# Performance work log

Hardware: AMD Instinct MI355X
Metric: run time of the kernel (lower is better)

The kernel has to match this reference:

```python
import jax, jax.numpy as jnp
import numpy as np

# Model dims (ViT-Base @ 384)
L, H, D, HD, M, P, IMG, B, NC, CH = 12, 12, 768, 64, 3072, 16, 384, 32, 1000, 3
NPATCH = (IMG // P) ** 2  # 576
SCALE = 1.0 / np.sqrt(HD)


def setup_inputs() -> dict:
    key = jax.random.key(0)
    ks = iter(jax.random.split(key, 16))
    def n(shape, s=0.02):
        return (jax.random.normal(next(ks), shape, jnp.float32) * s).astype(jnp.float32)
    return dict(
        x=jax.random.normal(next(ks), (B, CH, IMG, IMG), jnp.float32),
        conv_w=n((D, CH, P, P)), conv_b=jnp.zeros((D,), jnp.float32),
        cls_token=jnp.zeros((1, 1, D), jnp.float32),
        pos_emb=n((1, NPATCH + 1, D), 1.0),
        ln1_g=jnp.ones((L, D), jnp.float32), ln1_b=jnp.zeros((L, D), jnp.float32),
        wqkv=n((L, H, D, 3 * HD)), bqkv=jnp.zeros((L, H, 3 * HD), jnp.float32),
        wmsa=n((L, D, D)), bmsa=jnp.zeros((L, D), jnp.float32),
        ln2_g=jnp.ones((L, D), jnp.float32), ln2_b=jnp.zeros((L, D), jnp.float32),
        lnm_g=jnp.ones((L, D), jnp.float32), lnm_b=jnp.zeros((L, D), jnp.float32),
        w1=n((L, D, M)), b1=jnp.zeros((L, M), jnp.float32),
        w2=n((L, M, D)), b2=jnp.zeros((L, D), jnp.float32),
        lnf_g=jnp.ones((D,), jnp.float32), lnf_b=jnp.zeros((D,), jnp.float32),
        whead=n((D, NC)), bhead=jnp.zeros((NC,), jnp.float32),
    )


def _ln(x, g, b, eps=1e-5):
    mu = jnp.mean(x, axis=-1, keepdims=True)
    var = jnp.mean(jnp.square(x - mu), axis=-1, keepdims=True)
    return (x - mu) * jax.lax.rsqrt(var + eps) * g + b


def _encoder_block(x, p):
    (ln1_g, ln1_b, wqkv, bqkv, wmsa, bmsa,
     ln2_g, ln2_b, lnm_g, lnm_b, w1, b1, w2, b2) = p
    b = x.shape[0]
    h = _ln(x, ln1_g, ln1_b)
    # batched per-head QKV (math identical to looping over H small Linears)
    qkv = jnp.einsum('bsd,hde->bhse', h, wqkv) + bqkv[:, None, :]  # [B,H,S,3*HD]
    q, k, v = jnp.split(qkv, 3, axis=-1)
    attn = jax.nn.softmax(jnp.einsum('bhqe,bhke->bhqk', q, k) * SCALE, axis=-1)
    o = jnp.einsum('bhqk,bhke->bhqe', attn, v)          # [B,H,S,HD]
    o = o.transpose(0, 2, 1, 3).reshape(b, -1, D)        # concat heads along feature
    msa = jnp.einsum('bsd,de->bse', o, wmsa) + bmsa
    x1 = h + msa                                          # residual around MSA (post-LN1)
    h2 = _ln(x1, ln2_g, ln2_b)
    h2 = _ln(h2, lnm_g, lnm_b)                            # MLPBlock's own LayerNorm (double LN, faithful)
    mlp = jnp.einsum('bsm,md->bsd', jax.nn.gelu(jnp.einsum('bsd,dm->bsm', h2, w1) + b1, approximate=False), w2) + b2
    return x1 + mlp, None


def reference(x, conv_w, conv_b, cls_token, pos_emb,
              ln1_g, ln1_b, wqkv, bqkv, wmsa, bmsa,
              ln2_g, ln2_b, lnm_g, lnm_b, w1, b1, w2, b2,
              lnf_g, lnf_b, whead, bhead):
    b = x.shape[0]
    # patchify conv (image divisible by patch, so F.pad is a no-op)
    t = jax.lax.conv_general_dilated(x, conv_w, (P, P), 'VALID',
                                     dimension_numbers=('NCHW', 'OIHW', 'NCHW'))
    t = t + conv_b[None, :, None, None]
    # faithful to torch .view(b, -1, embed_dim) on NCHW layout (channel-major flatten)
    t = t.reshape(b, -1, D)
    n = t.shape[1]
    t = jnp.concatenate([jnp.broadcast_to(cls_token, (b, 1, D)), t], axis=1)
    t = t + pos_emb[:, :n + 1]
    stacked = (ln1_g, ln1_b, wqkv, bqkv, wmsa, bmsa,
               ln2_g, ln2_b, lnm_g, lnm_b, w1, b1, w2, b2)
    t, _ = jax.lax.scan(_encoder_block, t, stacked)
    y = _ln(t[:, 0], lnf_g, lnf_b)
    y = jax.nn.softmax(jnp.einsum('bd,dc->bc', y, whead) + bhead, axis=-1)
    return y
```

## Files before the change

### kernel.cpp

```cpp
#include <hip/hip_runtime.h>

using f16   = _Float16;
using f16x8 = __attribute__((ext_vector_type(8))) _Float16;
using f32x4 = __attribute__((ext_vector_type(4))) float;

#define MPAD  18560
#define MREAL 18464
#define MCONV 18432
#define SEQ   577
#define SPAD  640
#define NHEAD 12
#define NBATCH 32
#define SCALE_ 0.125f

__device__ __forceinline__ void load_lds16(const void* g, void* l) {
  __builtin_amdgcn_global_load_lds(
      (const __attribute__((address_space(1))) void*)g,
      (__attribute__((address_space(3))) void*)l, 16, 0, 0);
}

template<int K, int EPI>
__global__ __launch_bounds__(256) void gemm_k(
    const f16* __restrict__ A, const f16* __restrict__ Bt,
    const float* __restrict__ bias, const float* __restrict__ res,
    float* __restrict__ o32, f16* __restrict__ o16a, f16* __restrict__ o16b,
    f16* __restrict__ o16c, const float* __restrict__ pos, int N, int Mreal)
{
  __shared__ __align__(16) f16 As[128*32];
  __shared__ __align__(16) f16 Bs[128*32];
  const int tid = threadIdx.x;
  const int lane = tid & 63, wv = tid >> 6;
  const int bm = blockIdx.y << 7, bn = blockIdx.x << 7;
  const int wm = (wv >> 1) << 6, wn = (wv & 1) << 6;
  const int r16 = lane & 15, g4 = lane >> 4;
  const f32x4 Z4 = {0.f, 0.f, 0.f, 0.f};

  f32x4 acc[4][4];
#pragma unroll
  for (int m = 0; m < 4; ++m)
#pragma unroll
    for (int n = 0; n < 4; ++n) acc[m][n] = Z4;

  const int soff = wv * 1024 + lane * 8;
  for (int k0 = 0; k0 < K; k0 += 32) {
#pragma unroll
    for (int j = 0; j < 2; ++j) {
      int off = soff + j * 512;
      int row = off >> 5;
      int cs  = (off >> 3) & 3;
      int gc  = cs ^ (row & 3);
      load_lds16(A  + (size_t)(bm + row) * K + k0 + gc * 8, As + (wv*2 + j) * 512);
      load_lds16(Bt + (size_t)(bn + row) * K + k0 + gc * 8, Bs + (wv*2 + j) * 512);
    }
    __syncthreads();
    f16x8 af[4], bf[4];
#pragma unroll
    for (int m = 0; m < 4; ++m) {
      int row = wm + m * 16 + r16;
      af[m] = *(const f16x8*)(As + row * 32 + ((g4 ^ (row & 3)) << 3));
    }
#pragma unroll
    for (int n = 0; n < 4; ++n) {
      int row = wn + n * 16 + r16;
      bf[n] = *(const f16x8*)(Bs + row * 32 + ((g4 ^ (row & 3)) << 3));
    }
#pragma unroll
    for (int m = 0; m < 4; ++m)
#pragma unroll
      for (int n = 0; n < 4; ++n)
        acc[m][n] = __builtin_amdgcn_mfma_f32_16x16x32_f16(af[m], bf[n], acc[m][n], 0, 0, 0);
    __syncthreads();
  }

#pragma unroll
  for (int m = 0; m < 4; ++m) {
#pragma unroll
    for (int n = 0; n < 4; ++n) {
#pragma unroll
      for (int r = 0; r < 4; ++r) {
        int grow = bm + wm + m * 16 + g4 * 4 + r;
        int gcol = bn + wn + n * 16 + r16;
        float v = acc[m][n][r];
        if constexpr (EPI == 0) {
          if (grow < Mreal) {
            int b = grow / 576, p = grow - b * 576;
            int i = gcol * 576 + p;
            int sp = i / 768, dd = i - sp * 768;
            o32[((size_t)(b * SEQ + sp + 1)) * 768 + dd] =
                v + bias[gcol] + pos[(size_t)(sp + 1) * 768 + dd];
          }
        } else if constexpr (EPI == 1) {
          if (grow < Mreal) {
            int b = grow / SEQ, s = grow - b * SEQ;
            int hq = gcol / 192, rem = gcol - hq * 192;
            int sel = rem >> 6, e = rem & 63;
            float val = v + bias[gcol];
            int bh = b * NHEAD + hq;
            if (sel == 0)      o16a[((size_t)bh * SPAD + s) * 64 + e] = (f16)val;
            else if (sel == 1) o16b[((size_t)bh * SPAD + s) * 64 + e] = (f16)val;
            else               o16c[((size_t)bh * 64 + e) * SPAD + s] = (f16)val;
          }
        } else if constexpr (EPI == 2) {
          size_t idx = (size_t)grow * N + gcol;
          o32[idx] = v + bias[gcol] + res[idx];
        } else {
          float val = v + bias[gcol];
          float gl = 0.5f * val * (1.0f + erff(val * 0.70710678f));
          o16a[(size_t)grow * N + gcol] = (f16)gl;
        }
      }
    }
  }
}

__device__ __forceinline__ void block_red2(float& a, float& b, float* sm, int tid) {
  __syncthreads();
#pragma unroll
  for (int d = 32; d; d >>= 1) { a += __shfl_down(a, d); b += __shfl_down(b, d); }
  if ((tid & 63) == 0) { int w = tid >> 6; sm[w] = a; sm[w + 4] = b; }
  __syncthreads();
  a = sm[0] + sm[1] + sm[2] + sm[3];
  b = sm[4] + sm[5] + sm[6] + sm[7];
}

__global__ __launch_bounds__(256) void ln_fwd(const float* __restrict__ X,
    const float* __restrict__ g, const float* __restrict__ bb,
    float* __restrict__ ho, f16* __restrict__ hh)
{
  int row = blockIdx.x, tid = threadIdx.x;
  const float* x = X + (size_t)row * 768;
  float v0 = x[tid], v1 = x[tid + 256], v2 = x[tid + 512];
  float s = v0 + v1 + v2, s2 = v0*v0 + v1*v1 + v2*v2;
  __shared__ float sm[8];
  block_red2(s, s2, sm, tid);
  float mu = s * (1.f/768.f);
  float var = s2 * (1.f/768.f) - mu * mu;
  float rs = rsqrtf(var + 1e-5f);
  size_t base = (size_t)row * 768;
  float y0 = (v0 - mu) * rs * g[tid      ] + bb[tid      ];
  float y1 = (v1 - mu) * rs * g[tid + 256] + bb[tid + 256];
  float y2 = (v2 - mu) * rs * g[tid + 512] + bb[tid + 512];
  ho[base + tid] = y0; ho[base + tid + 256] = y1; ho[base + tid + 512] = y2;
  hh[base + tid] = (f16)y0; hh[base + tid + 256] = (f16)y1; hh[base + tid + 512] = (f16)y2;
}

__global__ __launch_bounds__(256) void ln2_fwd(const float* __restrict__ X,
    const float* __restrict__ g2, const float* __restrict__ bb2,
    const float* __restrict__ gm, const float* __restrict__ bbm,
    f16* __restrict__ hh)
{
  int row = blockIdx.x, tid = threadIdx.x;
  const float* x = X + (size_t)row * 768;
  float v0 = x[tid], v1 = x[tid + 256], v2 = x[tid + 512];
  float s = v0 + v1 + v2, s2 = v0*v0 + v1*v1 + v2*v2;
  __shared__ float sm[8];
  block_red2(s, s2, sm, tid);
  float mu = s * (1.f/768.f), var = s2 * (1.f/768.f) - mu * mu;
  float rs = rsqrtf(var + 1e-5f);
  float y0 = (v0 - mu) * rs * g2[tid      ] + bb2[tid      ];
  float y1 = (v1 - mu) * rs * g2[tid + 256] + bb2[tid + 256];
  float y2 = (v2 - mu) * rs * g2[tid + 512] + bb2[tid + 512];
  s = y0 + y1 + y2; s2 = y0*y0 + y1*y1 + y2*y2;
  block_red2(s, s2, sm, tid);
  mu = s * (1.f/768.f); var = s2 * (1.f/768.f) - mu * mu;
  rs = rsqrtf(var + 1e-5f);
  size_t base = (size_t)row * 768;
  hh[base + tid      ] = (f16)((y0 - mu) * rs * gm[tid      ] + bbm[tid      ]);
  hh[base + tid + 256] = (f16)((y1 - mu) * rs * gm[tid + 256] + bbm[tid + 256]);
  hh[base + tid + 512] = (f16)((y2 - mu) * rs * gm[tid + 512] + bbm[tid + 512]);
}

__global__ __launch_bounds__(256) void attn_k(const f16* __restrict__ qbuf,
    const f16* __restrict__ kbuf, const f16* __restrict__ vtbuf,
    f16* __restrict__ obuf)
{
  const int bh = blockIdx.y;
  const int b = bh / NHEAD, hd = bh - b * NHEAD;
  const int s0 = blockIdx.x << 6;
  const int tid = threadIdx.x, lane = tid & 63, wv = tid >> 6;
  const int r16 = lane & 15, g4 = lane >> 4;
  const f16* Q  = qbuf  + (size_t)bh * SPAD * 64;
  const f16* Kg = kbuf  + (size_t)bh * SPAD * 64;
  const f16* Vg = vtbuf + (size_t)bh * 64 * SPAD;
  __shared__ __align__(16) f16 Kt[64 * 64];
  __shared__ __align__(16) f16 Vt[64 * 64];
  __shared__ __align__(16) f16 Pw[4][16][72];
  const f32x4 Z4 = {0.f, 0.f, 0.f, 0.f};

  f16x8 qf[2];
  {
    const f16* qr = Q + (size_t)(s0 + wv * 16 + r16) * 64;
    qf[0] = *(const f16x8*)(qr + g4 * 8);
    qf[1] = *(const f16x8*)(qr + 32 + g4 * 8);
  }
  float m_run[4] = {-1e30f, -1e30f, -1e30f, -1e30f};
  float l_run[4] = {0.f, 0.f, 0.f, 0.f};
  f32x4 o_acc[4];
#pragma unroll
  for (int n = 0; n < 4; ++n) o_acc[n] = Z4;

  for (int kt = 0; kt < SPAD; kt += 64) {
#pragma unroll
    for (int j = 0; j < 2; ++j) {
      int off = (wv * 2 + j) * 1024 + lane * 16;
      int row = off >> 7;
      int cs  = (off >> 4) & 7;
      int gc  = cs ^ (row & 7);
      load_lds16(Kg + (size_t)(kt + row) * 64 + gc * 8, (void*)((char*)Kt + (wv*2 + j) * 1024));
      load_lds16(Vg + (size_t)row * SPAD + kt + gc * 8, (void*)((char*)Vt + (wv*2 + j) * 1024));
    }
    __syncthreads();

    f32x4 sa[4];
#pragma unroll
    for (int n = 0; n < 4; ++n) sa[n] = Z4;
#pragma unroll
    for (int n = 0; n < 4; ++n) {
      int krow = n * 16 + r16;
#pragma unroll
      for (int kc = 0; kc < 2; ++kc) {
        f16x8 kf = *(const f16x8*)(Kt + krow * 64 + (((kc * 4 + g4) ^ (krow & 7)) << 3));
        sa[n] = __builtin_amdgcn_mfma_f32_16x16x32_f16(qf[kc], kf, sa[n], 0, 0, 0);
      }
    }
#pragma unroll
    for (int r = 0; r < 4; ++r) {
      float mx = -1e30f;
#pragma unroll
      for (int n = 0; n < 4; ++n) {
        int key = kt + n * 16 + r16;
        float sv = (key < SEQ) ? sa[n][r] * SCALE_ : -1e30f;
        sa[n][r] = sv;
        mx = fmaxf(mx, sv);
      }
#pragma unroll
      for (int d = 1; d < 16; d <<= 1) mx = fmaxf(mx, __shfl_xor(mx, d));
      float mnew = fmaxf(m_run[r], mx);
      float alpha = __expf(m_run[r] - mnew);
      m_run[r] = mnew;
      float ssum = 0.f;
#pragma unroll
      for (int n = 0; n < 4; ++n) {
        float p = __expf(sa[n][r] - mnew);
        ssum += p;
        Pw[wv][g4 * 4 + r][n * 16 + r16] = (f16)p;
      }
#pragma unroll
      for (int d = 1; d < 16; d <<= 1) ssum += __shfl_xor(ssum, d);
      l_run[r] = l_run[r] * alpha + ssum;
#pragma unroll
      for (int n = 0; n < 4; ++n) o_acc[n][r] *= alpha;
    }
    f16x8 pf[2];
    pf[0] = *(const f16x8*)(&Pw[wv][r16][g4 * 8]);
    pf[1] = *(const f16x8*)(&Pw[wv][r16][32 + g4 * 8]);
#pragma unroll
    for (int n = 0; n < 4; ++n) {
      int erow = n * 16 + r16;
#pragma unroll
      for (int kc = 0; kc < 2; ++kc) {
        f16x8 vf = *(const f16x8*)(Vt + erow * 64 + (((kc * 4 + g4) ^ (erow & 7)) << 3));
        o_acc[n] = __builtin_amdgcn_mfma_f32_16x16x32_f16(pf[kc], vf, o_acc[n], 0, 0, 0);
      }
    }
    __syncthreads();
  }
  float inv[4];
#pragma unroll
  for (int r = 0; r < 4; ++r) inv[r] = 1.f / l_run[r];
#pragma unroll
  for (int n = 0; n < 4; ++n)
#pragma unroll
    for (int r = 0; r < 4; ++r) {
      int s = s0 + wv * 16 + g4 * 4 + r;
      if (s < SEQ)
        obuf[((size_t)(b * SEQ + s)) * 768 + hd * 64 + n * 16 + r16] =
            (f16)(o_acc[n][r] * inv[r]);
    }
}

__global__ __launch_bounds__(256) void cvt_transpose(const float* __restrict__ in,
    f16* __restrict__ out, int K, int N)
{
  __shared__ float t[32][33];
  int n0 = blockIdx.x << 5, k0 = blockIdx.y << 5;
  int tx = threadIdx.x & 31, ty = threadIdx.x >> 5;
#pragma unroll
  for (int i = 0; i < 4; ++i) t[ty + 8*i][tx] = in[(size_t)(k0 + ty + 8*i) * N + n0 + tx];
  __syncthreads();
#pragma unroll
  for (int i = 0; i < 4; ++i) out[(size_t)(n0 + ty + 8*i) * K + k0 + tx] = (f16)t[tx][ty + 8*i];
}

__global__ __launch_bounds__(256) void cvt_qkvw(const float* __restrict__ in, f16* __restrict__ out)
{
  __shared__ float t[32][33];
  int n0 = blockIdx.x << 5, k0 = blockIdx.y << 5;
  int tx = threadIdx.x & 31, ty = threadIdx.x >> 5;
  int hq = n0 / 192, r0 = n0 - hq * 192;
#pragma unroll
  for (int i = 0; i < 4; ++i)
    t[ty + 8*i][tx] = in[(size_t)hq * 147456 + (size_t)(k0 + ty + 8*i) * 192 + r0 + tx];
  __syncthreads();
#pragma unroll
  for (int i = 0; i < 4; ++i) out[(size_t)(n0 + ty + 8*i) * 768 + k0 + tx] = (f16)t[tx][ty + 8*i];
}

__global__ __launch_bounds__(256) void cvt_plain(const float* __restrict__ in,
    f16* __restrict__ out, int n)
{
  int i = blockIdx.x * 1024 + threadIdx.x;
#pragma unroll
  for (int j = 0; j < 4; ++j) { int idx = i + j * 256; if (idx < n) out[idx] = (f16)in[idx]; }
}

__global__ __launch_bounds__(256) void zero_vpad(f16* __restrict__ vtb) {
  int bh = blockIdx.x;
  for (int idx = threadIdx.x; idx < 64 * (SPAD - SEQ); idx += 256) {
    int e = idx / (SPAD - SEQ), s = SEQ + idx - e * (SPAD - SEQ);
    vtb[((size_t)bh * 64 + e) * SPAD + s] = (f16)0.f;
  }
}

__global__ __launch_bounds__(256) void im2col_k(const float* __restrict__ x, f16* __restrict__ out) {
  int row = blockIdx.x;
  int b = row / 576, p = row - b * 576;
  int py = p / 24, px = p - py * 24;
  int tid = threadIdx.x;
#pragma unroll
  for (int j = 0; j < 3; ++j) {
    int k = tid + j * 256;
    int c = k >> 8, rem = k & 255;
    int iy = rem >> 4, ix = rem & 15;
    out[(size_t)row * 768 + k] =
        (f16)x[(((size_t)(b * 3 + c)) * 384 + py * 16 + iy) * 384 + px * 16 + ix];
  }
}

__global__ __launch_bounds__(256) void cls_k(const float* __restrict__ ct,
    const float* __restrict__ pos, float* __restrict__ X)
{
  int b = blockIdx.x, tid = threadIdx.x;
#pragma unroll
  for (int j = 0; j < 3; ++j) {
    int d0 = tid + j * 256;
    X[((size_t)b * SEQ) * 768 + d0] = ct[d0] + pos[d0];
  }
}

__global__ __launch_bounds__(256) void head_k(const float* __restrict__ X,
    const float* __restrict__ g, const float* __restrict__ bb,
    const float* __restrict__ W, const float* __restrict__ bhd,
    float* __restrict__ out)
{
  int b = blockIdx.x, tid = threadIdx.x;
  const float* x = X + (size_t)(b * SEQ) * 768;
  float v0 = x[tid], v1 = x[tid + 256], v2 = x[tid + 512];
  float s = v0 + v1 + v2, s2 = v0*v0 + v1*v1 + v2*v2;
  __shared__ float sm[8];
  block_red2(s, s2, sm, tid);
  float mu = s * (1.f/768.f), var = s2 * (1.f/768.f) - mu * mu;
  float rs = rsqrtf(var + 1e-5f);
  __shared__ float y[768];
  y[tid      ] = (v0 - mu) * rs * g[tid      ] + bb[tid      ];
  y[tid + 256] = (v1 - mu) * rs * g[tid + 256] + bb[tid + 256];
  y[tid + 512] = (v2 - mu) * rs * g[tid + 512] + bb[tid + 512];
  __syncthreads();
  float lg[4];
#pragma unroll
  for (int j = 0; j < 4; ++j) {
    int c = tid + j * 256;
    float acc = (c < 1000) ? bhd[c] : -1e30f;
    if (c < 1000)
      for (int d = 0; d < 768; ++d) acc = fmaf(y[d], W[(size_t)d * 1000 + c], acc);
    lg[j] = acc;
  }
  float mx = fmaxf(fmaxf(lg[0], lg[1]), fmaxf(lg[2], lg[3]));
#pragma unroll
  for (int d = 32; d; d >>= 1) mx = fmaxf(mx, __shfl_down(mx, d));
  if ((tid & 63) == 0) sm[tid >> 6] = mx;
  __syncthreads();
  mx = fmaxf(fmaxf(sm[0], sm[1]), fmaxf(sm[2], sm[3]));
  float ex[4], se = 0.f;
#pragma unroll
  for (int j = 0; j < 4; ++j) {
    int c = tid + j * 256;
    ex[j] = (c < 1000) ? __expf(lg[j] - mx) : 0.f;
    se += ex[j];
  }
  __syncthreads();
#pragma unroll
  for (int d = 32; d; d >>= 1) se += __shfl_down(se, d);
  if ((tid & 63) == 0) sm[tid >> 6] = se;
  __syncthreads();
  se = sm[0] + sm[1] + sm[2] + sm[3];
  float inv = 1.f / se;
#pragma unroll
  for (int j = 0; j < 4; ++j) {
    int c = tid + j * 256;
    if (c < 1000) out[(size_t)b * 1000 + c] = ex[j] * inv;
  }
}

extern "C" void kernel_launch(void* const* d_in, const int* in_sizes, int n_in,
                              void* d_out, int out_size, void* d_ws, size_t ws_size,
                              hipStream_t stream)
{
  (void)in_sizes; (void)n_in; (void)out_size;
  const float* x      = (const float*)d_in[0];
  const float* conv_w = (const float*)d_in[1];
  const float* conv_b = (const float*)d_in[2];
  const float* cls_t  = (const float*)d_in[3];
  const float* pos    = (const float*)d_in[4];
  const float* ln1_g  = (const float*)d_in[5];
  const float* ln1_b  = (const float*)d_in[6];
  const float* wqkv   = (const float*)d_in[7];
  const float* bqkv   = (const float*)d_in[8];
  const float* wmsa   = (const float*)d_in[9];
  const float* bmsa   = (const float*)d_in[10];
  const float* ln2_g  = (const float*)d_in[11];
  const float* ln2_b  = (const float*)d_in[12];
  const float* lnm_g  = (const float*)d_in[13];
  const float* lnm_b  = (const float*)d_in[14];
  const float* w1     = (const float*)d_in[15];
  const float* b1     = (const float*)d_in[16];
  const float* w2     = (const float*)d_in[17];
  const float* b2     = (const float*)d_in[18];
  const float* lnf_g  = (const float*)d_in[19];
  const float* lnf_b  = (const float*)d_in[20];
  const float* whead  = (const float*)d_in[21];
  const float* bhead  = (const float*)d_in[22];
  float* out = (float*)d_out;

  char* wsp = (char*)d_ws;
  size_t off = 0;
  auto alloc = [&](size_t bytes) {
    char* p = wsp + off; off += (bytes + 255) & ~(size_t)255; return p;
  };
  float* X    = (float*)alloc((size_t)MPAD * 768 * 4);
  float* hbf  = (float*)alloc((size_t)MPAD * 768 * 4);
  f16*   hh   = (f16*)  alloc((size_t)MPAD * 768 * 2);
  f16*   abuf = (f16*)  alloc((size_t)MPAD * 3072 * 2);
  f16*   qb   = (f16*)  alloc((size_t)NBATCH * NHEAD * SPAD * 64 * 2);
  f16*   kb   = (f16*)  alloc((size_t)NBATCH * NHEAD * SPAD * 64 * 2);
  f16*   vtb  = (f16*)  alloc((size_t)NBATCH * NHEAD * SPAD * 64 * 2);
  f16*   WqkvT= (f16*)  alloc((size_t)2304 * 768 * 2);
  f16*   WmsaT= (f16*)  alloc((size_t)768 * 768 * 2);
  f16*   W1T  = (f16*)  alloc((size_t)3072 * 768 * 2);
  f16*   W2T  = (f16*)  alloc((size_t)768 * 3072 * 2);
  f16*   WcT  = (f16*)  alloc((size_t)768 * 768 * 2);
  f16*   obuf   = abuf;
  f16*   patchA = abuf;
  f16*   h2h    = hh;
  if (ws_size < off) return;

  zero_vpad<<<dim3(NBATCH * NHEAD), 256, 0, stream>>>(vtb);
  cvt_plain<<<dim3((768 * 768 + 1023) / 1024), 256, 0, stream>>>(conv_w, WcT, 768 * 768);
  im2col_k<<<dim3(MCONV), 256, 0, stream>>>(x, patchA);
  gemm_k<768, 0><<<dim3(6, 145), 256, 0, stream>>>(
      patchA, WcT, conv_b, nullptr, X, nullptr, nullptr, nullptr, pos, 768, MCONV);
  cls_k<<<dim3(NBATCH), 256, 0, stream>>>(cls_t, pos, X);

  for (int l = 0; l < 12; ++l) {
    cvt_qkvw<<<dim3(72, 24), 256, 0, stream>>>(wqkv + (size_t)l * 12 * 768 * 192, WqkvT);
    cvt_transpose<<<dim3(24, 24), 256, 0, stream>>>(wmsa + (size_t)l * 768 * 768, WmsaT, 768, 768);
    cvt_transpose<<<dim3(96, 24), 256, 0, stream>>>(w1 + (size_t)l * 768 * 3072, W1T, 768, 3072);
    cvt_transpose<<<dim3(24, 96), 256, 0, stream>>>(w2 + (size_t)l * 3072 * 768, W2T, 3072, 768);

    ln_fwd<<<dim3(MREAL), 256, 0, stream>>>(X, ln1_g + l * 768, ln1_b + l * 768, hbf, hh);
    gemm_k<768, 1><<<dim3(18, 145), 256, 0, stream>>>(
        hh, WqkvT, bqkv + (size_t)l * 2304, nullptr, nullptr, qb, kb, vtb, nullptr, 2304, MREAL);
    attn_k<<<dim3(10, NBATCH * NHEAD), 256, 0, stream>>>(qb, kb, vtb, obuf);
    gemm_k<768, 2><<<dim3(6, 145), 256, 0, stream>>>(
        obuf, WmsaT, bmsa + l * 768, hbf, X, nullptr, nullptr, nullptr, nullptr, 768, MREAL);
    ln2_fwd<<<dim3(MREAL), 256, 0, stream>>>(
        X, ln2_g + l * 768, ln2_b + l * 768, lnm_g + l * 768, lnm_b + l * 768, h2h);
    gemm_k<768, 3><<<dim3(24, 145), 256, 0, stream>>>(
        h2h, W1T, b1 + (size_t)l * 3072, nullptr, nullptr, abuf, nullptr, nullptr, nullptr, 3072, MREAL);
    gemm_k<3072, 2><<<dim3(6, 145), 256, 0, stream>>>(
        abuf, W2T, b2 + l * 768, X, X, nullptr, nullptr, nullptr, nullptr, 768, MREAL);
  }
  head_k<<<dim3(NBATCH), 256, 0, stream>>>(X, lnf_g, lnf_b, whead, bhead, out);
}
```

Baseline: 8.554 ms.

## Double-buffer LDS tiles in GEMM and attention, add XCD-aware block remap

Both the GEMM and the flash-attention kernels now use two LDS buffers, so the asynchronous global-to-LDS load of the next K tile is issued while the current tile is being computed, with one barrier per tile instead of two. Workgroup IDs are remapped so that consecutive tiles land on the same XCD, which is meant to improve L2 reuse. The GEMM swizzle gains an extra XOR term to reduce LDS bank conflicts, and the attention mask check is skipped on full tiles. LDS usage per block doubles, which may reduce occupancy.

Result: slower. 9.285 ms (+8.5%).

```diff
diff --git a/kernel.cpp b/kernel.cpp
--- a/kernel.cpp
+++ b/kernel.cpp
@@ -19,6 +19,12 @@
       (__attribute__((address_space(3))) void*)l, 16, 0, 0);
 }
 
+#define SYNC_PIPE() do {                                   \
+    asm volatile("s_waitcnt vmcnt(0)" ::: "memory");       \
+    __builtin_amdgcn_s_barrier();                          \
+    asm volatile("" ::: "memory");                         \
+  } while (0)
+
 template<int K, int EPI>
 __global__ __launch_bounds__(256) void gemm_k(
     const f16* __restrict__ A, const f16* __restrict__ Bt,
@@ -26,11 +32,22 @@
     float* __restrict__ o32, f16* __restrict__ o16a, f16* __restrict__ o16b,
     f16* __restrict__ o16c, const float* __restrict__ pos, int N, int Mreal)
 {
-  __shared__ __align__(16) f16 As[128*32];
-  __shared__ __align__(16) f16 Bs[128*32];
+  static_assert(K % 64 == 0, "NT must be even");
+  __shared__ __align__(16) f16 As[2][128 * 32];
+  __shared__ __align__(16) f16 Bs[2][128 * 32];
   const int tid = threadIdx.x;
   const int lane = tid & 63, wv = tid >> 6;
-  const int bm = blockIdx.y << 7, bn = blockIdx.x << 7;
+
+  const int gx = gridDim.x, gy = gridDim.y;
+  const int nwg = gx * gy;
+  const int flat = blockIdx.y * gx + blockIdx.x;
+  const int xcd = flat & 7;
+  const int qq = nwg >> 3, rr = nwg & 7;
+  const int pos_ = ((xcd < rr) ? xcd * (qq + 1) : rr * (qq + 1) + (xcd - rr) * qq)
+                   + (flat >> 3);
+  const int bxi = pos_ / gy, byi = pos_ - bxi * gy;
+  const int bm = byi << 7, bn = bxi << 7;
+
   const int wm = (wv >> 1) << 6, wn = (wv & 1) << 6;
   const int r16 = lane & 15, g4 = lane >> 4;
   const f32x4 Z4 = {0.f, 0.f, 0.f, 0.f};
@@ -41,35 +58,50 @@
 #pragma unroll
     for (int n = 0; n < 4; ++n) acc[m][n] = Z4;
 
-  const int soff = wv * 1024 + lane * 8;
-  for (int k0 = 0; k0 < K; k0 += 32) {
+  auto stage = [&](f16* Asd, f16* Bsd, int k0) {
 #pragma unroll
     for (int j = 0; j < 2; ++j) {
-      int off = soff + j * 512;
+      int off = wv * 1024 + j * 512 + lane * 8;
       int row = off >> 5;
       int cs  = (off >> 3) & 3;
-      int gc  = cs ^ (row & 3);
-      load_lds16(A  + (size_t)(bm + row) * K + k0 + gc * 8, As + (wv*2 + j) * 512);
-      load_lds16(Bt + (size_t)(bn + row) * K + k0 + gc * 8, Bs + (wv*2 + j) * 512);
-    }
-    __syncthreads();
+      int gc  = cs ^ (row & 3) ^ ((row >> 2) & 3);
+      load_lds16(A  + (size_t)(bm + row) * K + k0 + gc * 8, Asd + wv * 1024 + j * 512);
+      load_lds16(Bt + (size_t)(bn + row) * K + k0 + gc * 8, Bsd + wv * 1024 + j * 512);
+    }
+  };
+
+  auto compute = [&](const f16* As_, const f16* Bs_) {
     f16x8 af[4], bf[4];
 #pragma unroll
     for (int m = 0; m < 4; ++m) {
       int row = wm + m * 16 + r16;
-      af[m] = *(const f16x8*)(As + row * 32 + ((g4 ^ (row & 3)) << 3));
+      int sl = g4 ^ (row & 3) ^ ((row >> 2) & 3);
+      af[m] = *(const f16x8*)(As_ + row * 32 + (sl << 3));
     }
 #pragma unroll
     for (int n = 0; n < 4; ++n) {
       int row = wn + n * 16 + r16;
-      bf[n] = *(const f16x8*)(Bs + row * 32 + ((g4 ^ (row & 3)) << 3));
+      int sl = g4 ^ (row & 3) ^ ((row >> 2) & 3);
+      bf[n] = *(const f16x8*)(Bs_ + row * 32 + (sl << 3));
     }
 #pragma unroll
     for (int m = 0; m < 4; ++m)
 #pragma unroll
       for (int n = 0; n < 4; ++n)
         acc[m][n] = __builtin_amdgcn_mfma_f32_16x16x32_f16(af[m], bf[n], acc[m][n], 0, 0, 0);
-    __syncthreads();
+  };
+
+  constexpr int NT = K / 32;
+  stage(As[0], Bs[0], 0);
+  SYNC_PIPE();
+#pragma unroll 1
+  for (int t = 0; t < NT; t += 2) {
+    stage(As[1], Bs[1], (t + 1) * 32);
+    compute(As[0], Bs[0]);
+    SYNC_PIPE();
+    if (t + 2 < NT) stage(As[0], Bs[0], (t + 2) * 32);
+    compute(As[1], Bs[1]);
+    SYNC_PIPE();
   }
 
 #pragma unroll
@@ -174,16 +206,24 @@
     const f16* __restrict__ kbuf, const f16* __restrict__ vtbuf,
     f16* __restrict__ obuf)
 {
-  const int bh = blockIdx.y;
+  const int gx = gridDim.x;
+  const int nwg = gx * gridDim.y;
+  const int flat = blockIdx.y * gx + blockIdx.x;
+  const int xcd = flat & 7;
+  const int qq = nwg >> 3, rr = nwg & 7;
+  const int pos_ = ((xcd < rr) ? xcd * (qq + 1) : rr * (qq + 1) + (xcd - rr) * qq)
+                   + (flat >> 3);
+  const int bh = pos_ / gx;
+  const int s0 = (pos_ - bh * gx) << 6;
+
   const int b = bh / NHEAD, hd = bh - b * NHEAD;
-  const int s0 = blockIdx.x << 6;
   const int tid = threadIdx.x, lane = tid & 63, wv = tid >> 6;
   const int r16 = lane & 15, g4 = lane >> 4;
   const f16* Q  = qbuf  + (size_t)bh * SPAD * 64;
   const f16* Kg = kbuf  + (size_t)bh * SPAD * 64;
   const f16* Vg = vtbuf + (size_t)bh * 64 * SPAD;
-  __shared__ __align__(16) f16 Kt[64 * 64];
-  __shared__ __align__(16) f16 Vt[64 * 64];
+  __shared__ __align__(16) f16 Kt[2][64 * 64];
+  __shared__ __align__(16) f16 Vt[2][64 * 64];
   __shared__ __align__(16) f16 Pw[4][16][72];
   const f32x4 Z4 = {0.f, 0.f, 0.f, 0.f};
 
@@ -199,18 +239,20 @@
 #pragma unroll
   for (int n = 0; n < 4; ++n) o_acc[n] = Z4;
 
-  for (int kt = 0; kt < SPAD; kt += 64) {
+  auto stagekv = [&](f16* Ktd, f16* Vtd, int kt) {
 #pragma unroll
     for (int j = 0; j < 2; ++j) {
       int off = (wv * 2 + j) * 1024 + lane * 16;
       int row = off >> 7;
       int cs  = (off >> 4) & 7;
       int gc  = cs ^ (row & 7);
-      load_lds16(Kg + (size_t)(kt + row) * 64 + gc * 8, (void*)((char*)Kt + (wv*2 + j) * 1024));
-      load_lds16(Vg + (size_t)row * SPAD + kt + gc * 8, (void*)((char*)Vt + (wv*2 + j) * 1024));
-    }
-    __syncthreads();
-
+      load_lds16(Kg + (size_t)(kt + row) * 64 + gc * 8, (char*)Ktd + (wv*2 + j) * 1024);
+      load_lds16(Vg + (size_t)row * SPAD + kt + gc * 8, (char*)Vtd + (wv*2 + j) * 1024);
+    }
+  };
+
+  auto tile_compute = [&](const f16* Kt_, const f16* Vt_, int kt) {
+    const bool fullt = (kt + 64 <= SEQ);
     f32x4 sa[4];
 #pragma unroll
     for (int n = 0; n < 4; ++n) sa[n] = Z4;
@@ -219,7 +261,7 @@
       int krow = n * 16 + r16;
 #pragma unroll
       for (int kc = 0; kc < 2; ++kc) {
-        f16x8 kf = *(const f16x8*)(Kt + krow * 64 + (((kc * 4 + g4) ^ (krow & 7)) << 3));
+        f16x8 kf = *(const f16x8*)(Kt_ + krow * 64 + (((kc * 4 + g4) ^ (krow & 7)) << 3));
         sa[n] = __builtin_amdgcn_mfma_f32_16x16x32_f16(qf[kc], kf, sa[n], 0, 0, 0);
       }
     }
@@ -228,8 +270,8 @@
       float mx = -1e30f;
 #pragma unroll
       for (int n = 0; n < 4; ++n) {
-        int key = kt + n * 16 + r16;
-        float sv = (key < SEQ) ? sa[n][r] * SCALE_ : -1e30f;
+        float sv = sa[n][r] * SCALE_;
+        if (!fullt && (kt + n * 16 + r16 >= SEQ)) sv = -1e30f;
         sa[n][r] = sv;
         mx = fmaxf(mx, sv);
       }
@@ -259,12 +301,24 @@
       int erow = n * 16 + r16;
 #pragma unroll
       for (int kc = 0; kc < 2; ++kc) {
-        f16x8 vf = *(const f16x8*)(Vt + erow * 64 + (((kc * 4 + g4) ^ (erow & 7)) << 3));
+        f16x8 vf = *(const f16x8*)(Vt_ + erow * 64 + (((kc * 4 + g4) ^ (erow & 7)) << 3));
         o_acc[n] = __builtin_amdgcn_mfma_f32_16x16x32_f16(pf[kc], vf, o_acc[n], 0, 0, 0);
       }
     }
-    __syncthreads();
-  }
+  };
+
+  stagekv(Kt[0], Vt[0], 0);
+  SYNC_PIPE();
+#pragma unroll 1
+  for (int kt = 0; kt < SPAD; kt += 128) {
+    stagekv(Kt[1], Vt[1], kt + 64);
+    tile_compute(Kt[0], Vt[0], kt);
+    SYNC_PIPE();
+    if (kt + 128 < SPAD) stagekv(Kt[0], Vt[0], kt + 128);
+    tile_compute(Kt[1], Vt[1], kt + 64);
+    SYNC_PIPE();
+  }
+
   float inv[4];
 #pragma unroll
   for (int r = 0; r < 4; ++r) inv[r] = 1.f / l_run[r];
```

## Double GEMM K-tile to 64, remap blocks per XCD, hoist weight conversion

Applied to the files above, without the earlier changes.

The GEMM kernel now stages 64-wide K slices with an 8-way XOR swizzle, which halves the barrier count per K loop. Workgroup IDs are remapped so neighbouring tiles land on the same XCD, aiming for better L2 reuse. When the workspace is large enough, all 12 layers' weights are converted and transposed up front in single batched launches instead of four launches per layer. The patch-embed GEMM grid also drops its unused padding row of tiles. The costs are double the LDS per block, which may lower occupancy, and a larger workspace footprint.

After: 9.352 ms. 1.09x slower.

```diff
diff --git a/kernel.cpp b/kernel.cpp
--- a/kernel.cpp
+++ b/kernel.cpp
@@ -26,11 +26,22 @@
     float* __restrict__ o32, f16* __restrict__ o16a, f16* __restrict__ o16b,
     f16* __restrict__ o16c, const float* __restrict__ pos, int N, int Mreal)
 {
-  __shared__ __align__(16) f16 As[128*32];
-  __shared__ __align__(16) f16 Bs[128*32];
+  static_assert(K % 64 == 0, "BK=64");
+  __shared__ __align__(16) f16 As[128 * 64];
+  __shared__ __align__(16) f16 Bs[128 * 64];
   const int tid = threadIdx.x;
   const int lane = tid & 63, wv = tid >> 6;
-  const int bm = blockIdx.y << 7, bn = blockIdx.x << 7;
+
+  const int gx = gridDim.x, gy = gridDim.y;
+  const int nwg = gx * gy;
+  const int flat = blockIdx.y * gx + blockIdx.x;
+  const int xcd = flat & 7;
+  const int qq = nwg >> 3, rr = nwg & 7;
+  const int pos_ = ((xcd < rr) ? xcd * (qq + 1) : rr * (qq + 1) + (xcd - rr) * qq)
+                   + (flat >> 3);
+  const int bxi = pos_ / gy, byi = pos_ - bxi * gy;
+  const int bm = byi << 7, bn = bxi << 7;
+
   const int wm = (wv >> 1) << 6, wn = (wv & 1) << 6;
   const int r16 = lane & 15, g4 = lane >> 4;
   const f32x4 Z4 = {0.f, 0.f, 0.f, 0.f};
@@ -41,34 +52,36 @@
 #pragma unroll
     for (int n = 0; n < 4; ++n) acc[m][n] = Z4;
 
-  const int soff = wv * 1024 + lane * 8;
-  for (int k0 = 0; k0 < K; k0 += 32) {
-#pragma unroll
-    for (int j = 0; j < 2; ++j) {
-      int off = soff + j * 512;
-      int row = off >> 5;
-      int cs  = (off >> 3) & 3;
-      int gc  = cs ^ (row & 3);
-      load_lds16(A  + (size_t)(bm + row) * K + k0 + gc * 8, As + (wv*2 + j) * 512);
-      load_lds16(Bt + (size_t)(bn + row) * K + k0 + gc * 8, Bs + (wv*2 + j) * 512);
+  const int srow = lane >> 3;
+  const int sgc  = (lane & 7) ^ srow;
+
+  for (int k0 = 0; k0 < K; k0 += 64) {
+#pragma unroll
+    for (int j = 0; j < 4; ++j) {
+      int rb = (wv * 4 + j) * 8;
+      load_lds16(A  + (size_t)(bm + rb + srow) * K + k0 + sgc * 8, As + (wv * 4 + j) * 512);
+      load_lds16(Bt + (size_t)(bn + rb + srow) * K + k0 + sgc * 8, Bs + (wv * 4 + j) * 512);
     }
     __syncthreads();
-    f16x8 af[4], bf[4];
-#pragma unroll
-    for (int m = 0; m < 4; ++m) {
-      int row = wm + m * 16 + r16;
-      af[m] = *(const f16x8*)(As + row * 32 + ((g4 ^ (row & 3)) << 3));
-    }
-#pragma unroll
-    for (int n = 0; n < 4; ++n) {
-      int row = wn + n * 16 + r16;
-      bf[n] = *(const f16x8*)(Bs + row * 32 + ((g4 ^ (row & 3)) << 3));
-    }
-#pragma unroll
-    for (int m = 0; m < 4; ++m)
-#pragma unroll
-      for (int n = 0; n < 4; ++n)
-        acc[m][n] = __builtin_amdgcn_mfma_f32_16x16x32_f16(af[m], bf[n], acc[m][n], 0, 0, 0);
+#pragma unroll
+    for (int ks = 0; ks < 2; ++ks) {
+      f16x8 af[4], bf[4];
+#pragma unroll
+      for (int m = 0; m < 4; ++m) {
+        int row = wm + m * 16 + r16;
+        af[m] = *(const f16x8*)(As + row * 64 + ((((ks << 2) | g4) ^ (row & 7)) << 3));
+      }
+#pragma unroll
+      for (int n = 0; n < 4; ++n) {
+        int row = wn + n * 16 + r16;
+        bf[n] = *(const f16x8*)(Bs + row * 64 + ((((ks << 2) | g4) ^ (row & 7)) << 3));
+      }
+#pragma unroll
+      for (int m = 0; m < 4; ++m)
+#pragma unroll
+        for (int n = 0; n < 4; ++n)
+          acc[m][n] = __builtin_amdgcn_mfma_f32_16x16x32_f16(af[m], bf[n], acc[m][n], 0, 0, 0);
+    }
     __syncthreads();
   }
 
@@ -280,8 +293,10 @@
 }
 
 __global__ __launch_bounds__(256) void cvt_transpose(const float* __restrict__ in,
-    f16* __restrict__ out, int K, int N)
-{
+    f16* __restrict__ out, int K, int N, size_t ls_in, size_t ls_out)
+{
+  in  += (size_t)blockIdx.z * ls_in;
+  out += (size_t)blockIdx.z * ls_out;
   __shared__ float t[32][33];
   int n0 = blockIdx.x << 5, k0 = blockIdx.y << 5;
   int tx = threadIdx.x & 31, ty = threadIdx.x >> 5;
@@ -292,8 +307,11 @@
   for (int i = 0; i < 4; ++i) out[(size_t)(n0 + ty + 8*i) * K + k0 + tx] = (f16)t[tx][ty + 8*i];
 }
 
-__global__ __launch_bounds__(256) void cvt_qkvw(const float* __restrict__ in, f16* __restrict__ out)
-{
+__global__ __launch_bounds__(256) void cvt_qkvw(const float* __restrict__ in,
+    f16* __restrict__ out, size_t ls_in, size_t ls_out)
+{
+  in  += (size_t)blockIdx.z * ls_in;
+  out += (size_t)blockIdx.z * ls_out;
   __shared__ float t[32][33];
   int n0 = blockIdx.x << 5, k0 = blockIdx.y << 5;
   int tx = threadIdx.x & 31, ty = threadIdx.x >> 5;
@@ -432,6 +450,18 @@
   const float* bhead  = (const float*)d_in[22];
   float* out = (float*)d_out;
 
+  const size_t szQ  = (size_t)2304 * 768;
+  const size_t szM  = (size_t)768 * 768;
+  const size_t szW1 = (size_t)3072 * 768;
+  const size_t szW2 = (size_t)768 * 3072;
+  const size_t fixed_bytes =
+      (size_t)MPAD * 768 * 4 + (size_t)MPAD * 768 * 4 + (size_t)MPAD * 768 * 2 +
+      (size_t)MPAD * 3072 * 2 + 3 * ((size_t)NBATCH * NHEAD * SPAD * 64 * 2) +
+      (size_t)768 * 768 * 2  + 16 * 256 ;
+  const bool hoist =
+      ws_size >= fixed_bytes + 12 * (szQ + szM + szW1 + szW2) * 2 + 8 * 256;
+  const int LW = hoist ? 12 : 1;
+
   char* wsp = (char*)d_ws;
   size_t off = 0;
   auto alloc = [&](size_t bytes) {
@@ -444,11 +474,11 @@
   f16*   qb   = (f16*)  alloc((size_t)NBATCH * NHEAD * SPAD * 64 * 2);
   f16*   kb   = (f16*)  alloc((size_t)NBATCH * NHEAD * SPAD * 64 * 2);
   f16*   vtb  = (f16*)  alloc((size_t)NBATCH * NHEAD * SPAD * 64 * 2);
-  f16*   WqkvT= (f16*)  alloc((size_t)2304 * 768 * 2);
-  f16*   WmsaT= (f16*)  alloc((size_t)768 * 768 * 2);
-  f16*   W1T  = (f16*)  alloc((size_t)3072 * 768 * 2);
-  f16*   W2T  = (f16*)  alloc((size_t)768 * 3072 * 2);
   f16*   WcT  = (f16*)  alloc((size_t)768 * 768 * 2);
+  f16*   WqkvT= (f16*)  alloc(LW * szQ  * 2);
+  f16*   WmsaT= (f16*)  alloc(LW * szM  * 2);
+  f16*   W1T  = (f16*)  alloc(LW * szW1 * 2);
+  f16*   W2T  = (f16*)  alloc(LW * szW2 * 2);
   f16*   obuf   = abuf;
   f16*   patchA = abuf;
   f16*   h2h    = hh;
@@ -456,29 +486,45 @@
 
   zero_vpad<<<dim3(NBATCH * NHEAD), 256, 0, stream>>>(vtb);
   cvt_plain<<<dim3((768 * 768 + 1023) / 1024), 256, 0, stream>>>(conv_w, WcT, 768 * 768);
+  if (hoist) {
+    cvt_qkvw<<<dim3(72, 24, 12), 256, 0, stream>>>(wqkv, WqkvT, (size_t)12*768*192, szQ);
+    cvt_transpose<<<dim3(24, 24, 12), 256, 0, stream>>>(wmsa, WmsaT, 768, 768, szM, szM);
+    cvt_transpose<<<dim3(96, 24, 12), 256, 0, stream>>>(w1, W1T, 768, 3072, szW1, szW1);
+    cvt_transpose<<<dim3(24, 96, 12), 256, 0, stream>>>(w2, W2T, 3072, 768, szW2, szW2);
+  }
   im2col_k<<<dim3(MCONV), 256, 0, stream>>>(x, patchA);
-  gemm_k<768, 0><<<dim3(6, 145), 256, 0, stream>>>(
+  gemm_k<768, 0><<<dim3(6, 144), 256, 0, stream>>>(
       patchA, WcT, conv_b, nullptr, X, nullptr, nullptr, nullptr, pos, 768, MCONV);
   cls_k<<<dim3(NBATCH), 256, 0, stream>>>(cls_t, pos, X);
 
   for (int l = 0; l < 12; ++l) {
-    cvt_qkvw<<<dim3(72, 24), 256, 0, stream>>>(wqkv + (size_t)l * 12 * 768 * 192, WqkvT);
-    cvt_transpose<<<dim3(24, 24), 256, 0, stream>>>(wmsa + (size_t)l * 768 * 768, WmsaT, 768, 768);
-    cvt_transpose<<<dim3(96, 24), 256, 0, stream>>>(w1 + (size_t)l * 768 * 3072, W1T, 768, 3072);
-    cvt_transpose<<<dim3(24, 96), 256, 0, stream>>>(w2 + (size_t)l * 3072 * 768, W2T, 3072, 768);
+    f16* wq  = WqkvT + (hoist ? (size_t)l * szQ  : 0);
+    f16* wms = WmsaT + (hoist ? (size_t)l * szM  : 0);
+    f16* w1t = W1T   + (hoist ? (size_t)l * szW1 : 0);
+    f16* w2t = W2T   + (hoist ? (size_t)l * szW2 : 0);
+    if (!hoist) {
+      cvt_qkvw<<<dim3(72, 24), 256, 0, stream>>>(
+          wqkv + (size_t)l * 12 * 768 * 192, wq, 0, 0);
+      cvt_transpose<<<dim3(24, 24), 256, 0, stream>>>(
+          wmsa + (size_t)l * 768 * 768, wms, 768, 768, 0, 0);
+      cvt_transpose<<<dim3(96, 24), 256, 0, stream>>>(
+          w1 + (size_t)l * 768 * 3072, w1t, 768, 3072, 0, 0);
+      cvt_transpose<<<dim3(24, 96), 256, 0, stream>>>(
+          w2 + (size_t)l * 3072 * 768, w2t, 3072, 768, 0, 0);
+    }
 
     ln_fwd<<<dim3(MREAL), 256, 0, stream>>>(X, ln1_g + l * 768, ln1_b + l * 768, hbf, hh);
     gemm_k<768, 1><<<dim3(18, 145), 256, 0, stream>>>(
-        hh, WqkvT, bqkv + (size_t)l * 2304, nullptr, nullptr, qb, kb, vtb, nullptr, 2304, MREAL);
+        hh, wq, bqkv + (size_t)l * 2304, nullptr, nullptr, qb, kb, vtb, nullptr, 2304, MREAL);
     attn_k<<<dim3(10, NBATCH * NHEAD), 256, 0, stream>>>(qb, kb, vtb, obuf);
     gemm_k<768, 2><<<dim3(6, 145), 256, 0, stream>>>(
-        obuf, WmsaT, bmsa + l * 768, hbf, X, nullptr, nullptr, nullptr, nullptr, 768, MREAL);
+        obuf, wms, bmsa + l * 768, hbf, X, nullptr, nullptr, nullptr, nullptr, 768, MREAL);
     ln2_fwd<<<dim3(MREAL), 256, 0, stream>>>(
         X, ln2_g + l * 768, ln2_b + l * 768, lnm_g + l * 768, lnm_b + l * 768, h2h);
     gemm_k<768, 3><<<dim3(24, 145), 256, 0, stream>>>(
-        h2h, W1T, b1 + (size_t)l * 3072, nullptr, nullptr, abuf, nullptr, nullptr, nullptr, 3072, MREAL);
+        h2h, w1t, b1 + (size_t)l * 3072, nullptr, nullptr, abuf, nullptr, nullptr, nullptr, 3072, MREAL);
     gemm_k<3072, 2><<<dim3(6, 145), 256, 0, stream>>>(
-        abuf, W2T, b2 + l * 768, X, X, nullptr, nullptr, nullptr, nullptr, 768, MREAL);
+        abuf, w2t, b2 + l * 768, X, X, nullptr, nullptr, nullptr, nullptr, 768, MREAL);
   }
   head_k<<<dim3(NBATCH), 256, 0, stream>>>(X, lnf_g, lnf_b, whead, bhead, out);
 }
```
